# Performance work log

Measured on AMD Instinct MI355X. Metric: run time of the kernel, lower is better.

Reference implementation:

```python
import jax, jax.numpy as jnp
import numpy as np

DIM = 1024
NUM_HEADS = 16
HEAD_D = DIM // NUM_HEADS


def setup_inputs() -> dict:
    key = jax.random.key(0)
    ks = jax.random.split(key, 9)
    B, T, D = 4, 2048, DIM
    s = 1.0 / np.sqrt(D)
    return {
        "x": jax.random.normal(ks[0], (B, T, D), dtype=jnp.float32),
        "Wq": jax.random.normal(ks[1], (D, D), dtype=jnp.float32) * s,
        "bq": jnp.zeros((D,), dtype=jnp.float32),
        "Wk": jax.random.normal(ks[2], (D, D), dtype=jnp.float32) * s,
        "bk": jnp.zeros((D,), dtype=jnp.float32),
        "Wv": jax.random.normal(ks[3], (D, D), dtype=jnp.float32) * s,
        "bv": jnp.zeros((D,), dtype=jnp.float32),
        "Wo": jax.random.normal(ks[4], (D, D), dtype=jnp.float32) * s,
        "bo": jnp.zeros((D,), dtype=jnp.float32),
    }


def reference(x, Wq, bq, Wk, bk, Wv, bv, Wo, bo):
    B, T, D = x.shape
    H, Hd = NUM_HEADS, HEAD_D
    # QKV projections (torch Linear: x @ W.T + b)
    q = (x @ Wq.T + bq).reshape(B, T, H, Hd).transpose(0, 2, 1, 3)  # [B,H,T,Hd]
    k = (x @ Wk.T + bk).reshape(B, T, H, Hd).transpose(0, 2, 1, 3)
    v = (x @ Wv.T + bv).reshape(B, T, H, Hd).transpose(0, 2, 1, 3)
    scores = jnp.einsum("bhqd,bhkd->bhqk", q, k) / jnp.sqrt(jnp.float32(Hd))
    probs = jax.nn.softmax(scores, axis=-1)
    out = jnp.einsum("bhqk,bhkd->bhqd", probs, v)  # [B,H,T,Hd]
    out = out.transpose(0, 2, 1, 3).reshape(B, T, D)
    return out @ Wo.T + bo
```

## Files before the change

### kernel.cpp

```cpp
#include <hip/hip_runtime.h>

typedef unsigned short u16;
typedef unsigned int   u32;
typedef __bf16 bf16;
typedef __attribute__((ext_vector_type(8))) __bf16 bf16x8;
typedef __attribute__((ext_vector_type(4))) float  f32x4;


__device__ __forceinline__ u16 f2bf(float f) {
  u32 u = __float_as_uint(f);
  u32 r = (u + 0x7fffu + ((u >> 16) & 1u)) >> 16;
  return (u16)r;
}

__device__ __forceinline__ void gload_lds16(const void* g, void* l) {
  __builtin_amdgcn_global_load_lds((__attribute__((address_space(1))) u32*)g,
                                   (__attribute__((address_space(3))) u32*)l,
                                   16, 0, 0);
}

__device__ __forceinline__ u32 cvt_pk_bf16(float lo, float hi) {
  u32 r;
  asm("v_cvt_pk_bf16_f32 %0, %1, %2" : "=v"(r) : "v"(lo), "v"(hi));
  return r;
}

#define SCL_LOG2E 0.1803368801111204f


__global__ __launch_bounds__(256) void cvt_bf16_kernel(const float* __restrict__ in,
                                                       u16* __restrict__ out, int n4) {
  int i = blockIdx.x * blockDim.x + threadIdx.x;
  int stride = gridDim.x * blockDim.x;
  for (; i < n4; i += stride) {
    float4 v = ((const float4*)in)[i];
    uint2 o;
    o.x = (u32)f2bf(v.x) | ((u32)f2bf(v.y) << 16);
    o.y = (u32)f2bf(v.z) | ((u32)f2bf(v.w) << 16);
    ((uint2*)out)[i] = o;
  }
}

__global__ __launch_bounds__(256) void cvt4_kernel(const float* __restrict__ p0,
                                                   const float* __restrict__ p1,
                                                   const float* __restrict__ p2,
                                                   const float* __restrict__ p3,
                                                   u16* o0, u16* o1, u16* o2, u16* o3) {
  const int which = blockIdx.x >> 8;
  const float* in = which == 0 ? p0 : which == 1 ? p1 : which == 2 ? p2 : p3;
  u16* out = which == 0 ? o0 : which == 1 ? o1 : which == 2 ? o2 : o3;
  int i = (blockIdx.x & 255) * 256 + threadIdx.x;
  #pragma unroll
  for (int r = 0; r < 4; ++r, i += 65536) {
    float4 v = ((const float4*)in)[i];
    uint2 o;
    o.x = (u32)f2bf(v.x) | ((u32)f2bf(v.y) << 16);
    o.y = (u32)f2bf(v.z) | ((u32)f2bf(v.w) << 16);
    ((uint2*)out)[i] = o;
  }
}


#define GK 1024
#define GN 1024

__global__ __launch_bounds__(256) void gemm_qkv_kernel(const u16* __restrict__ A,
                                                       const u16* __restrict__ Wq,
                                                       const u16* __restrict__ Wk,
                                                       const u16* __restrict__ Wv,
                                                       const float* __restrict__ bq,
                                                       const float* __restrict__ bk,
                                                       const float* __restrict__ bv,
                                                       u16* __restrict__ Qo,
                                                       u16* __restrict__ Ko,
                                                       u16* __restrict__ Vo) {
  __shared__ u16 sA[2][128 * 32];
  __shared__ u16 sB[2][128 * 32];

  const int tid  = threadIdx.x;
  const int lane = tid & 63;
  const int w    = tid >> 6;
  const int wm   = w >> 1, wn = w & 1;
  const int lid  = (blockIdx.x & 7) * 192 + (blockIdx.x >> 3);
  const int which = lid >> 9;
  const int sub   = lid & 511;
  const u16*  W    = which == 0 ? Wq : which == 1 ? Wk : Wv;
  const float* bias = which == 0 ? bq : which == 1 ? bk : bv;
  const int tn   = sub & 7;
  const int tm   = sub >> 3;
  const int m0   = tm * 128, n0 = tn * 128;
  const int rgrp = lane >> 4, rlo = lane & 15;

  auto stage = [&](int buf, int kt) {
    int k0 = kt * 32;
    #pragma unroll
    for (int r = 0; r < 2; ++r) {
      int c   = (w * 2 + r) * 64 + lane;
      int row = c >> 2;
      int cb  = c & 3;
      int col = ((cb ^ (row & 3)) * 8);
      gload_lds16(A + (size_t)(m0 + row) * GK + k0 + col, &sA[buf][(w * 2 + r) * 512]);
      gload_lds16(W + (size_t)(n0 + row) * GK + k0 + col, &sB[buf][(w * 2 + r) * 512]);
    }
  };

  f32x4 acc[4][4] = {};

  stage(0, 0);
  asm volatile("s_waitcnt vmcnt(0)" ::: "memory");
  __syncthreads();

  for (int kt = 0; kt < GK / 32; ++kt) {
    int buf = kt & 1;
    if (kt + 1 < GK / 32) stage(buf ^ 1, kt + 1);

    bf16x8 a[4], b[4];
    #pragma unroll
    for (int i = 0; i < 4; ++i) {
      int row = wm * 64 + i * 16 + rlo;
      int cb  = rgrp ^ (row & 3);
      a[i] = *(const bf16x8*)&sA[buf][row * 32 + cb * 8];
    }
    #pragma unroll
    for (int j = 0; j < 4; ++j) {
      int row = wn * 64 + j * 16 + rlo;
      int cb  = rgrp ^ (row & 3);
      b[j] = *(const bf16x8*)&sB[buf][row * 32 + cb * 8];
    }
    #pragma unroll
    for (int i = 0; i < 4; ++i)
      #pragma unroll
      for (int j = 0; j < 4; ++j)
        acc[i][j] = __builtin_amdgcn_mfma_f32_16x16x32_bf16(a[i], b[j], acc[i][j], 0, 0, 0);

    asm volatile("s_waitcnt vmcnt(0)" ::: "memory");
    __syncthreads();
  }

  #pragma unroll
  for (int i = 0; i < 4; ++i) {
    #pragma unroll
    for (int j = 0; j < 4; ++j) {
      #pragma unroll
      for (int r = 0; r < 4; ++r) {
        int m = m0 + wm * 64 + i * 16 + rgrp * 4 + r;
        int n = n0 + wn * 64 + j * 16 + rlo;
        float v = acc[i][j][r] + bias[n];
        int b = m >> 11, t = m & 2047, h = n >> 6, hd = n & 63;
        if (which == 0) {
          Qo[(((size_t)(b * 16 + h) * 2048 + t) << 6) + hd] = (u16)__builtin_bit_cast(u16, (bf16)v);
        } else if (which == 1) {
          Ko[(((size_t)(b * 16 + h) * 2048 + t) << 6) + hd] =
              (u16)__builtin_bit_cast(u16, (bf16)(v * SCL_LOG2E));
        } else {
          Vo[((size_t)(b * 16 + h) * 64 + hd) * 2048 + t] = (u16)__builtin_bit_cast(u16, (bf16)v);
        }
      }
    }
  }
}

__global__ __launch_bounds__(256) void gemm_out_kernel(const u16* __restrict__ A,
                                                       const u16* __restrict__ W,
                                                       const float* __restrict__ bias,
                                                       float* __restrict__ Cout) {
  __shared__ u16 sA[2][128 * 32];
  __shared__ u16 sB[2][128 * 32];

  const int tid  = threadIdx.x;
  const int lane = tid & 63;
  const int w    = tid >> 6;
  const int wm   = w >> 1, wn = w & 1;
  const int lid  = (blockIdx.x & 7) * 64 + (blockIdx.x >> 3);
  const int tn   = lid & 7;
  const int tm   = lid >> 3;
  const int m0   = tm * 128, n0 = tn * 128;
  const int rgrp = lane >> 4, rlo = lane & 15;

  auto stage = [&](int buf, int kt) {
    int k0 = kt * 32;
    #pragma unroll
    for (int r = 0; r < 2; ++r) {
      int c   = (w * 2 + r) * 64 + lane;
      int row = c >> 2;
      int cb  = c & 3;
      int col = ((cb ^ (row & 3)) * 8);
      gload_lds16(A + (size_t)(m0 + row) * GK + k0 + col, &sA[buf][(w * 2 + r) * 512]);
      gload_lds16(W + (size_t)(n0 + row) * GK + k0 + col, &sB[buf][(w * 2 + r) * 512]);
    }
  };

  f32x4 acc[4][4] = {};

  stage(0, 0);
  asm volatile("s_waitcnt vmcnt(0)" ::: "memory");
  __syncthreads();

  for (int kt = 0; kt < GK / 32; ++kt) {
    int buf = kt & 1;
    if (kt + 1 < GK / 32) stage(buf ^ 1, kt + 1);

    bf16x8 a[4], b[4];
    #pragma unroll
    for (int i = 0; i < 4; ++i) {
      int row = wm * 64 + i * 16 + rlo;
      int cb  = rgrp ^ (row & 3);
      a[i] = *(const bf16x8*)&sA[buf][row * 32 + cb * 8];
    }
    #pragma unroll
    for (int j = 0; j < 4; ++j) {
      int row = wn * 64 + j * 16 + rlo;
      int cb  = rgrp ^ (row & 3);
      b[j] = *(const bf16x8*)&sB[buf][row * 32 + cb * 8];
    }
    #pragma unroll
    for (int i = 0; i < 4; ++i)
      #pragma unroll
      for (int j = 0; j < 4; ++j)
        acc[i][j] = __builtin_amdgcn_mfma_f32_16x16x32_bf16(a[i], b[j], acc[i][j], 0, 0, 0);

    asm volatile("s_waitcnt vmcnt(0)" ::: "memory");
    __syncthreads();
  }

  #pragma unroll
  for (int i = 0; i < 4; ++i)
    #pragma unroll
    for (int j = 0; j < 4; ++j)
      #pragma unroll
      for (int r = 0; r < 4; ++r) {
        int m = m0 + wm * 64 + i * 16 + rgrp * 4 + r;
        int n = n0 + wn * 64 + j * 16 + rlo;
        Cout[(size_t)m * GN + n] = acc[i][j][r] + bias[n];
      }
}


__global__ __launch_bounds__(256) void attn_kernel(const u16* __restrict__ Q,
                                                   const u16* __restrict__ K,
                                                   const u16* __restrict__ Vt,
                                                   bf16* __restrict__ O) {
  __shared__ u16 sK[2][64 * 64];
  __shared__ u16 sV[2][64 * 64];

  const int tid  = threadIdx.x;
  const int lane = tid & 63;
  const int w    = tid >> 6;
  const int rgrp = lane >> 4, rlo = lane & 15;
  const int bid  = (blockIdx.x & 7) * 128 + (blockIdx.x >> 3);
  const int qt   = bid & 15;
  const int bh   = bid >> 4;

  const u16* Qh = Q  + (size_t)bh * 2048 * 64;
  const u16* Kh = K  + (size_t)bh * 2048 * 64;
  const u16* Vh = Vt + (size_t)bh * 64 * 2048;

  auto stage = [&](int buf, int t) {
    #pragma unroll
    for (int r = 0; r < 2; ++r) {
      int c   = (w * 2 + r) * 64 + lane;
      int row = c >> 3;
      int cb  = c & 7;
      int col = (cb ^ (row & 7)) * 8;
      gload_lds16(Kh + ((size_t)(t * 64 + row)) * 64 + col, &sK[buf][(w * 2 + r) * 512]);
      gload_lds16(Vh + (size_t)row * 2048 + t * 64 + col,   &sV[buf][(w * 2 + r) * 512]);
    }
  };

  stage(0, 0);

  bf16x8 bQ[2][2];
  #pragma unroll
  for (int qg = 0; qg < 2; ++qg) {
    int q0 = qt * 128 + w * 32 + qg * 16 + rlo;
    bQ[qg][0] = *(const bf16x8*)&Qh[(size_t)q0 * 64 + rgrp * 8];
    bQ[qg][1] = *(const bf16x8*)&Qh[(size_t)q0 * 64 + 32 + rgrp * 8];
  }

  asm volatile("s_waitcnt vmcnt(0)" ::: "memory");
  __syncthreads();

  float lsum[2] = {0.f, 0.f};
  f32x4 o[2][4] = {};

  for (int t = 0; t < 32; ++t) {
    const int cur = t & 1;
    if (t + 1 < 32) stage(cur ^ 1, t + 1);

    f32x4 sT[2][4];
    #pragma unroll
    for (int nt = 0; nt < 4; ++nt) {
      sT[0][nt] = (f32x4){0.f, 0.f, 0.f, 0.f};
      sT[1][nt] = (f32x4){0.f, 0.f, 0.f, 0.f};
    }
    __builtin_amdgcn_s_setprio(1);
    #pragma unroll
    for (int nt = 0; nt < 4; ++nt)
      #pragma unroll
      for (int kk = 0; kk < 2; ++kk) {
        int row = nt * 16 + rlo;
        int cb  = (kk * 4 + rgrp) ^ (row & 7);
        bf16x8 aK = *(const bf16x8*)&sK[cur][row * 64 + cb * 8];
        sT[0][nt] = __builtin_amdgcn_mfma_f32_16x16x32_bf16(aK, bQ[0][kk], sT[0][nt], 0, 0, 0);
        sT[1][nt] = __builtin_amdgcn_mfma_f32_16x16x32_bf16(aK, bQ[1][kk], sT[1][nt], 0, 0, 0);
      }
    __builtin_amdgcn_s_setprio(0);

    #pragma unroll
    for (int qg = 0; qg < 2; ++qg) {
      #pragma unroll
      for (int nt = 0; nt < 4; ++nt)
        #pragma unroll
        for (int r = 0; r < 4; ++r)
          sT[qg][nt][r] = __builtin_amdgcn_exp2f(sT[qg][nt][r]);
      #pragma unroll
      for (int nt = 0; nt < 4; ++nt)
        lsum[qg] += (sT[qg][nt][0] + sT[qg][nt][1]) + (sT[qg][nt][2] + sT[qg][nt][3]);
    }

    bf16x8 bP[2][2];
    #pragma unroll
    for (int qg = 0; qg < 2; ++qg) {
      u32 pw[4][2];
      #pragma unroll
      for (int nt = 0; nt < 4; ++nt) {
        pw[nt][0] = cvt_pk_bf16(sT[qg][nt][0], sT[qg][nt][1]);
        pw[nt][1] = cvt_pk_bf16(sT[qg][nt][2], sT[qg][nt][3]);
      }
      #pragma unroll
      for (int kk = 0; kk < 2; ++kk) {
        u32 a0 = pw[2 * kk][0], b0 = pw[2 * kk + 1][0];
        u32 a1 = pw[2 * kk][1], b1 = pw[2 * kk + 1][1];
        asm("v_permlane32_swap_b32 %0, %1" : "+v"(a0), "+v"(b0));
        asm("v_permlane16_swap_b32 %0, %1" : "+v"(a0), "+v"(b0));
        asm("v_permlane32_swap_b32 %0, %1" : "+v"(a1), "+v"(b1));
        asm("v_permlane16_swap_b32 %0, %1" : "+v"(a1), "+v"(b1));
        union { u32 u[4]; bf16x8 v; } fu;
        fu.u[0] = a0; fu.u[1] = a1; fu.u[2] = b0; fu.u[3] = b1;
        bP[qg][kk] = fu.v;
      }
    }

    __builtin_amdgcn_s_setprio(1);
    #pragma unroll
    for (int kk = 0; kk < 2; ++kk)
      #pragma unroll
      for (int dt = 0; dt < 4; ++dt) {
        int rowv = dt * 16 + rlo;
        int cbv  = (kk * 4 + rgrp) ^ (rowv & 7);
        bf16x8 aV = *(const bf16x8*)&sV[cur][rowv * 64 + cbv * 8];
        o[0][dt] = __builtin_amdgcn_mfma_f32_16x16x32_bf16(aV, bP[0][kk], o[0][dt], 0, 0, 0);
        o[1][dt] = __builtin_amdgcn_mfma_f32_16x16x32_bf16(aV, bP[1][kk], o[1][dt], 0, 0, 0);
      }
    __builtin_amdgcn_s_setprio(0);

    asm volatile("s_waitcnt vmcnt(0)" ::: "memory");
    __syncthreads();
  }

  const int b = bh >> 4, h = bh & 15;
  #pragma unroll
  for (int qg = 0; qg < 2; ++qg) {
    float ls = lsum[qg];
    ls += __shfl_xor(ls, 16);
    ls += __shfl_xor(ls, 32);
    const float inv = 1.0f / ls;
    const int tq = qt * 128 + w * 32 + qg * 16 + rlo;
    #pragma unroll
    for (int dt = 0; dt < 4; ++dt) {
      uint2 st;
      st.x = cvt_pk_bf16(o[qg][dt][0] * inv, o[qg][dt][1] * inv);
      st.y = cvt_pk_bf16(o[qg][dt][2] * inv, o[qg][dt][3] * inv);
      *(uint2*)&O[((size_t)(b * 2048 + tq)) * 1024 + h * 64 + dt * 16 + rgrp * 4] = st;
    }
  }
}


extern "C" void kernel_launch(void* const* d_in, const int* in_sizes, int n_in,
                              void* d_out, int out_size, void* d_ws, size_t ws_size,
                              hipStream_t stream) {
  const float* x  = (const float*)d_in[0];
  const float* Wq = (const float*)d_in[1];
  const float* bq = (const float*)d_in[2];
  const float* Wk = (const float*)d_in[3];
  const float* bk = (const float*)d_in[4];
  const float* Wv = (const float*)d_in[5];
  const float* bv = (const float*)d_in[6];
  const float* Wo = (const float*)d_in[7];
  const float* bo = (const float*)d_in[8];

  char* ws = (char*)d_ws;
  u16* xb  = (u16*)(ws);
  u16* Wqb = (u16*)(ws + 16777216);
  u16* Wkb = (u16*)(ws + 18874368);
  u16* Wvb = (u16*)(ws + 20971520);
  u16* Wob = (u16*)(ws + 23068672);
  u16* Qb  = (u16*)(ws + 25165824);
  u16* Kb  = (u16*)(ws + 41943040);
  u16* Vtb = (u16*)(ws + 58720256);
  u16* Ab  = (u16*)(ws + 75497472);

  cvt_bf16_kernel<<<4096, 256, 0, stream>>>(x, xb, 8388608 / 4);
  cvt4_kernel<<<1024, 256, 0, stream>>>(Wq, Wk, Wv, Wo, Wqb, Wkb, Wvb, Wob);

  gemm_qkv_kernel<<<1536, 256, 0, stream>>>(xb, Wqb, Wkb, Wvb, bq, bk, bv, Qb, Kb, Vtb);

  attn_kernel<<<1024, 256, 0, stream>>>(Qb, Kb, Vtb, (bf16*)Ab);

  gemm_out_kernel<<<512, 256, 0, stream>>>(Ab, Wob, bo, (float*)d_out);
}
```

Measured before the change: 253.2 us.

## Load attention K/V fragments directly from global into registers, dropping LDS staging

The attention kernel no longer stages K and V tiles through double-buffered shared memory with barriers. Each wave loads its MFMA operand fragments straight from global memory into registers, using a two-deep register ping-pong that prefetches the next tile while the current one is computed. It also interleaves the softmax/P conversion with the PV MFMAs per query group. This removes LDS traffic and __syncthreads, but each of the 4 waves now fetches the same K/V data separately, relying on L1/L2 to absorb the redundancy, and register pressure rises.

```diff
diff --git a/kernel.cpp b/kernel.cpp
--- a/kernel.cpp
+++ b/kernel.cpp
@@ -240,9 +240,6 @@
                                                    const u16* __restrict__ K,
                                                    const u16* __restrict__ Vt,
                                                    bf16* __restrict__ O) {
-  __shared__ u16 sK[2][64 * 64];
-  __shared__ u16 sV[2][64 * 64];
-
   const int tid  = threadIdx.x;
   const int lane = tid & 63;
   const int w    = tid >> 6;
@@ -255,20 +252,6 @@
   const u16* Kh = K  + (size_t)bh * 2048 * 64;
   const u16* Vh = Vt + (size_t)bh * 64 * 2048;
 
-  auto stage = [&](int buf, int t) {
-    #pragma unroll
-    for (int r = 0; r < 2; ++r) {
-      int c   = (w * 2 + r) * 64 + lane;
-      int row = c >> 3;
-      int cb  = c & 7;
-      int col = (cb ^ (row & 7)) * 8;
-      gload_lds16(Kh + ((size_t)(t * 64 + row)) * 64 + col, &sK[buf][(w * 2 + r) * 512]);
-      gload_lds16(Vh + (size_t)row * 2048 + t * 64 + col,   &sV[buf][(w * 2 + r) * 512]);
-    }
-  };
-
-  stage(0, 0);
-
   bf16x8 bQ[2][2];
   #pragma unroll
   for (int qg = 0; qg < 2; ++qg) {
@@ -277,16 +260,27 @@
     bQ[qg][1] = *(const bf16x8*)&Qh[(size_t)q0 * 64 + 32 + rgrp * 8];
   }
 
-  asm volatile("s_waitcnt vmcnt(0)" ::: "memory");
-  __syncthreads();
-
   float lsum[2] = {0.f, 0.f};
   f32x4 o[2][4] = {};
 
-  for (int t = 0; t < 32; ++t) {
-    const int cur = t & 1;
-    if (t + 1 < 32) stage(cur ^ 1, t + 1);
-
+  auto loadK = [&](bf16x8 (&kf)[8], int t) {
+    #pragma unroll
+    for (int nt = 0; nt < 4; ++nt)
+      #pragma unroll
+      for (int kk = 0; kk < 2; ++kk)
+        kf[nt * 2 + kk] =
+            *(const bf16x8*)&Kh[(size_t)(t * 64 + nt * 16 + rlo) * 64 + kk * 32 + rgrp * 8];
+  };
+  auto loadV = [&](bf16x8 (&vf)[8], int t) {
+    #pragma unroll
+    for (int dt = 0; dt < 4; ++dt)
+      #pragma unroll
+      for (int kk = 0; kk < 2; ++kk)
+        vf[dt * 2 + kk] =
+            *(const bf16x8*)&Vh[(size_t)(dt * 16 + rlo) * 2048 + t * 64 + kk * 32 + rgrp * 8];
+  };
+
+  auto compute = [&](const bf16x8 (&kf)[8], const bf16x8 (&vf)[8]) {
     f32x4 sT[2][4];
     #pragma unroll
     for (int nt = 0; nt < 4; ++nt) {
@@ -298,11 +292,8 @@
     for (int nt = 0; nt < 4; ++nt)
       #pragma unroll
       for (int kk = 0; kk < 2; ++kk) {
-        int row = nt * 16 + rlo;
-        int cb  = (kk * 4 + rgrp) ^ (row & 7);
-        bf16x8 aK = *(const bf16x8*)&sK[cur][row * 64 + cb * 8];
-        sT[0][nt] = __builtin_amdgcn_mfma_f32_16x16x32_bf16(aK, bQ[0][kk], sT[0][nt], 0, 0, 0);
-        sT[1][nt] = __builtin_amdgcn_mfma_f32_16x16x32_bf16(aK, bQ[1][kk], sT[1][nt], 0, 0, 0);
+        sT[0][nt] = __builtin_amdgcn_mfma_f32_16x16x32_bf16(kf[nt * 2 + kk], bQ[0][kk], sT[0][nt], 0, 0, 0);
+        sT[1][nt] = __builtin_amdgcn_mfma_f32_16x16x32_bf16(kf[nt * 2 + kk], bQ[1][kk], sT[1][nt], 0, 0, 0);
       }
     __builtin_amdgcn_s_setprio(0);
 
@@ -316,17 +307,14 @@
       #pragma unroll
       for (int nt = 0; nt < 4; ++nt)
         lsum[qg] += (sT[qg][nt][0] + sT[qg][nt][1]) + (sT[qg][nt][2] + sT[qg][nt][3]);
-    }
-
-    bf16x8 bP[2][2];
-    #pragma unroll
-    for (int qg = 0; qg < 2; ++qg) {
+
       u32 pw[4][2];
       #pragma unroll
       for (int nt = 0; nt < 4; ++nt) {
         pw[nt][0] = cvt_pk_bf16(sT[qg][nt][0], sT[qg][nt][1]);
         pw[nt][1] = cvt_pk_bf16(sT[qg][nt][2], sT[qg][nt][3]);
       }
+      bf16x8 bP[2];
       #pragma unroll
       for (int kk = 0; kk < 2; ++kk) {
         u32 a0 = pw[2 * kk][0], b0 = pw[2 * kk + 1][0];
@@ -337,25 +325,26 @@
         asm("v_permlane16_swap_b32 %0, %1" : "+v"(a1), "+v"(b1));
         union { u32 u[4]; bf16x8 v; } fu;
         fu.u[0] = a0; fu.u[1] = a1; fu.u[2] = b0; fu.u[3] = b1;
-        bP[qg][kk] = fu.v;
+        bP[kk] = fu.v;
       }
-    }
-
-    __builtin_amdgcn_s_setprio(1);
-    #pragma unroll
-    for (int kk = 0; kk < 2; ++kk)
-      #pragma unroll
-      for (int dt = 0; dt < 4; ++dt) {
-        int rowv = dt * 16 + rlo;
-        int cbv  = (kk * 4 + rgrp) ^ (rowv & 7);
-        bf16x8 aV = *(const bf16x8*)&sV[cur][rowv * 64 + cbv * 8];
-        o[0][dt] = __builtin_amdgcn_mfma_f32_16x16x32_bf16(aV, bP[0][kk], o[0][dt], 0, 0, 0);
-        o[1][dt] = __builtin_amdgcn_mfma_f32_16x16x32_bf16(aV, bP[1][kk], o[1][dt], 0, 0, 0);
-      }
-    __builtin_amdgcn_s_setprio(0);
-
-    asm volatile("s_waitcnt vmcnt(0)" ::: "memory");
-    __syncthreads();
+
+      __builtin_amdgcn_s_setprio(1);
+      #pragma unroll
+      for (int kk = 0; kk < 2; ++kk)
+        #pragma unroll
+        for (int dt = 0; dt < 4; ++dt)
+          o[qg][dt] = __builtin_amdgcn_mfma_f32_16x16x32_bf16(vf[dt * 2 + kk], bP[kk], o[qg][dt], 0, 0, 0);
+      __builtin_amdgcn_s_setprio(0);
+    }
+  };
+
+  bf16x8 kfA[8], vfA[8], kfB[8], vfB[8];
+  loadK(kfA, 0); loadV(vfA, 0);
+  for (int t = 0; t < 32; t += 2) {
+    loadK(kfB, t + 1); loadV(vfB, t + 1);
+    compute(kfA, vfA);
+    if (t + 2 < 32) { loadK(kfA, t + 2); loadV(vfA, t + 2); }
+    compute(kfB, vfB);
   }
 
   const int b = bh >> 4, h = bh & 15;
```

After: 377.8 us. +49.2%, slower.

## Store Q/K row-major, vectorize V-transpose stores, compute softmax denominator via MFMA

Applied to the files above, without the earlier changes.

The QKV projection epilogue now writes Q and K in plain [B*T, D] row-major layout, which gives contiguous per-lane stores, and writes transposed V with packed 4-element stores instead of scalar ones. The attention kernel reads Q/K with a head stride of 1024 and precomputes its staging base pointers. The per-lane exp-sum reduction and cross-lane shuffles are replaced by an extra MFMA against a ones vector, so the denominator accumulates from the same bf16-rounded probabilities used for P·V. PV MFMAs are now interleaved per query group, which costs additional MFMA work in exchange for fewer VALU adds.

```diff
diff --git a/kernel.cpp b/kernel.cpp
--- a/kernel.cpp
+++ b/kernel.cpp
@@ -137,26 +137,34 @@
     __syncthreads();
   }
 
-  #pragma unroll
-  for (int i = 0; i < 4; ++i) {
-    #pragma unroll
-    for (int j = 0; j < 4; ++j) {
-      #pragma unroll
-      for (int r = 0; r < 4; ++r) {
-        int m = m0 + wm * 64 + i * 16 + rgrp * 4 + r;
-        int n = n0 + wn * 64 + j * 16 + rlo;
-        float v = acc[i][j][r] + bias[n];
-        int b = m >> 11, t = m & 2047, h = n >> 6, hd = n & 63;
-        if (which == 0) {
-          Qo[(((size_t)(b * 16 + h) * 2048 + t) << 6) + hd] = (u16)__builtin_bit_cast(u16, (bf16)v);
-        } else if (which == 1) {
-          Ko[(((size_t)(b * 16 + h) * 2048 + t) << 6) + hd] =
-              (u16)__builtin_bit_cast(u16, (bf16)(v * SCL_LOG2E));
-        } else {
-          Vo[((size_t)(b * 16 + h) * 64 + hd) * 2048 + t] = (u16)__builtin_bit_cast(u16, (bf16)v);
+  if (which <= 1) {
+    u16* out = which == 0 ? Qo : Ko;
+    const float scl = which == 0 ? 1.0f : SCL_LOG2E;
+    #pragma unroll
+    for (int i = 0; i < 4; ++i)
+      #pragma unroll
+      for (int j = 0; j < 4; ++j)
+        #pragma unroll
+        for (int r = 0; r < 4; ++r) {
+          int m = m0 + wm * 64 + i * 16 + rgrp * 4 + r;
+          int n = n0 + wn * 64 + j * 16 + rlo;
+          float v = (acc[i][j][r] + bias[n]) * scl;
+          out[(size_t)m * GN + n] = (u16)__builtin_bit_cast(u16, (bf16)v);
         }
-      }
-    }
+  } else {
+    #pragma unroll
+    for (int i = 0; i < 4; ++i)
+      #pragma unroll
+      for (int j = 0; j < 4; ++j) {
+        int mb = m0 + wm * 64 + i * 16 + rgrp * 4;
+        int n  = n0 + wn * 64 + j * 16 + rlo;
+        int b = mb >> 11, t = mb & 2047, h = n >> 6, hd = n & 63;
+        float bv_ = bias[n];
+        uint2 st;
+        st.x = cvt_pk_bf16(acc[i][j][0] + bv_, acc[i][j][1] + bv_);
+        st.y = cvt_pk_bf16(acc[i][j][2] + bv_, acc[i][j][3] + bv_);
+        *(uint2*)&Vo[((size_t)(b * 16 + h) * 64 + hd) * 2048 + t] = st;
+      }
   }
 }
 
@@ -250,21 +258,26 @@
   const int bid  = (blockIdx.x & 7) * 128 + (blockIdx.x >> 3);
   const int qt   = bid & 15;
   const int bh   = bid >> 4;
-
-  const u16* Qh = Q  + (size_t)bh * 2048 * 64;
-  const u16* Kh = K  + (size_t)bh * 2048 * 64;
+  const int b    = bh >> 4, h = bh & 15;
+
+  const u16* Qh = Q  + (size_t)b * 2048 * 1024 + h * 64;
+  const u16* Kh = K  + (size_t)b * 2048 * 1024 + h * 64;
   const u16* Vh = Vt + (size_t)bh * 64 * 2048;
 
+  const int c0 = (w * 2 + 0) * 64 + lane;
+  const int c1 = (w * 2 + 1) * 64 + lane;
+  const int r0 = c0 >> 3, col0 = ((c0 & 7) ^ (r0 & 7)) * 8;
+  const int r1 = c1 >> 3, col1 = ((c1 & 7) ^ (r1 & 7)) * 8;
+  const u16* kb0 = Kh + (size_t)r0 * 1024 + col0;
+  const u16* kb1 = Kh + (size_t)r1 * 1024 + col1;
+  const u16* vb0 = Vh + (size_t)r0 * 2048 + col0;
+  const u16* vb1 = Vh + (size_t)r1 * 2048 + col1;
+
   auto stage = [&](int buf, int t) {
-    #pragma unroll
-    for (int r = 0; r < 2; ++r) {
-      int c   = (w * 2 + r) * 64 + lane;
-      int row = c >> 3;
-      int cb  = c & 7;
-      int col = (cb ^ (row & 7)) * 8;
-      gload_lds16(Kh + ((size_t)(t * 64 + row)) * 64 + col, &sK[buf][(w * 2 + r) * 512]);
-      gload_lds16(Vh + (size_t)row * 2048 + t * 64 + col,   &sV[buf][(w * 2 + r) * 512]);
-    }
+    gload_lds16(kb0 + (size_t)t * 65536, &sK[buf][(w * 2 + 0) * 512]);
+    gload_lds16(kb1 + (size_t)t * 65536, &sK[buf][(w * 2 + 1) * 512]);
+    gload_lds16(vb0 + t * 64,            &sV[buf][(w * 2 + 0) * 512]);
+    gload_lds16(vb1 + t * 64,            &sV[buf][(w * 2 + 1) * 512]);
   };
 
   stage(0, 0);
@@ -273,14 +286,18 @@
   #pragma unroll
   for (int qg = 0; qg < 2; ++qg) {
     int q0 = qt * 128 + w * 32 + qg * 16 + rlo;
-    bQ[qg][0] = *(const bf16x8*)&Qh[(size_t)q0 * 64 + rgrp * 8];
-    bQ[qg][1] = *(const bf16x8*)&Qh[(size_t)q0 * 64 + 32 + rgrp * 8];
-  }
+    bQ[qg][0] = *(const bf16x8*)&Qh[(size_t)q0 * 1024 + rgrp * 8];
+    bQ[qg][1] = *(const bf16x8*)&Qh[(size_t)q0 * 1024 + 32 + rgrp * 8];
+  }
+
+  bf16x8 vones;
+  #pragma unroll
+  for (int i = 0; i < 8; ++i) vones[i] = (bf16)1.0f;
 
   asm volatile("s_waitcnt vmcnt(0)" ::: "memory");
   __syncthreads();
 
-  float lsum[2] = {0.f, 0.f};
+  f32x4 lden[2] = {};
   f32x4 o[2][4] = {};
 
   for (int t = 0; t < 32; ++t) {
@@ -313,20 +330,14 @@
         #pragma unroll
         for (int r = 0; r < 4; ++r)
           sT[qg][nt][r] = __builtin_amdgcn_exp2f(sT[qg][nt][r]);
-      #pragma unroll
-      for (int nt = 0; nt < 4; ++nt)
-        lsum[qg] += (sT[qg][nt][0] + sT[qg][nt][1]) + (sT[qg][nt][2] + sT[qg][nt][3]);
-    }
-
-    bf16x8 bP[2][2];
-    #pragma unroll
-    for (int qg = 0; qg < 2; ++qg) {
+
       u32 pw[4][2];
       #pragma unroll
       for (int nt = 0; nt < 4; ++nt) {
         pw[nt][0] = cvt_pk_bf16(sT[qg][nt][0], sT[qg][nt][1]);
         pw[nt][1] = cvt_pk_bf16(sT[qg][nt][2], sT[qg][nt][3]);
       }
+      bf16x8 bP[2];
       #pragma unroll
       for (int kk = 0; kk < 2; ++kk) {
         u32 a0 = pw[2 * kk][0], b0 = pw[2 * kk + 1][0];
@@ -337,34 +348,31 @@
         asm("v_permlane16_swap_b32 %0, %1" : "+v"(a1), "+v"(b1));
         union { u32 u[4]; bf16x8 v; } fu;
         fu.u[0] = a0; fu.u[1] = a1; fu.u[2] = b0; fu.u[3] = b1;
-        bP[qg][kk] = fu.v;
-      }
-    }
-
-    __builtin_amdgcn_s_setprio(1);
-    #pragma unroll
-    for (int kk = 0; kk < 2; ++kk)
-      #pragma unroll
-      for (int dt = 0; dt < 4; ++dt) {
-        int rowv = dt * 16 + rlo;
-        int cbv  = (kk * 4 + rgrp) ^ (rowv & 7);
-        bf16x8 aV = *(const bf16x8*)&sV[cur][rowv * 64 + cbv * 8];
-        o[0][dt] = __builtin_amdgcn_mfma_f32_16x16x32_bf16(aV, bP[0][kk], o[0][dt], 0, 0, 0);
-        o[1][dt] = __builtin_amdgcn_mfma_f32_16x16x32_bf16(aV, bP[1][kk], o[1][dt], 0, 0, 0);
-      }
-    __builtin_amdgcn_s_setprio(0);
+        bP[kk] = fu.v;
+      }
+
+      __builtin_amdgcn_s_setprio(1);
+      #pragma unroll
+      for (int kk = 0; kk < 2; ++kk) {
+        lden[qg] = __builtin_amdgcn_mfma_f32_16x16x32_bf16(vones, bP[kk], lden[qg], 0, 0, 0);
+        #pragma unroll
+        for (int dt = 0; dt < 4; ++dt) {
+          int rowv = dt * 16 + rlo;
+          int cbv  = (kk * 4 + rgrp) ^ (rowv & 7);
+          bf16x8 aV = *(const bf16x8*)&sV[cur][rowv * 64 + cbv * 8];
+          o[qg][dt] = __builtin_amdgcn_mfma_f32_16x16x32_bf16(aV, bP[kk], o[qg][dt], 0, 0, 0);
+        }
+      }
+      __builtin_amdgcn_s_setprio(0);
+    }
 
     asm volatile("s_waitcnt vmcnt(0)" ::: "memory");
     __syncthreads();
   }
 
-  const int b = bh >> 4, h = bh & 15;
   #pragma unroll
   for (int qg = 0; qg < 2; ++qg) {
-    float ls = lsum[qg];
-    ls += __shfl_xor(ls, 16);
-    ls += __shfl_xor(ls, 32);
-    const float inv = 1.0f / ls;
+    const float inv = 1.0f / lden[qg][0];
     const int tq = qt * 128 + w * 32 + qg * 16 + rlo;
     #pragma unroll
     for (int dt = 0; dt < 4; ++dt) {
```

New measurement: 226.8 us. -10.4%, faster.
